# Kernel tuning notes

Measured on AMD Instinct MI355X. Metric: run time of the kernel, lower is better.

The kernel has to match this reference:

```python
import jax, jax.numpy as jnp
import numpy as np

NEG_BIG = -9e15
LRELU_SLOPE = 0.2  # alpha

N = 8192
IN_F = 256
OUT_F = 128


def setup_inputs() -> dict:
    key = jax.random.key(0)
    k1, k2, k3, k4 = jax.random.split(key, 4)
    inputs = jax.random.normal(k1, (N, IN_F), dtype=jnp.float32)
    adj = jax.random.randint(k2, (N, N), 0, 2, dtype=jnp.int32)
    # xavier_uniform with gain=1.414
    gain = 1.414
    bW = gain * np.sqrt(6.0 / (IN_F + OUT_F))
    W = jax.random.uniform(k3, (IN_F, OUT_F), minval=-bW, maxval=bW, dtype=jnp.float32)
    ba = gain * np.sqrt(6.0 / (2 * OUT_F + 1))
    a = jax.random.uniform(k4, (2 * OUT_F, 1), minval=-ba, maxval=ba, dtype=jnp.float32)
    return {"inputs": inputs, "adj": adj, "W": W, "a": a}


def reference(inputs, adj, W, a):
    # h: [N, F']
    h = inputs @ W
    # a^T [h_i || h_j] = h_i . a[:F'] + h_j . a[F':]  -- avoids the O(N^2 * 2F') concat
    a1 = a[:OUT_F, 0]   # [F']
    a2 = a[OUT_F:, 0]   # [F']
    s1 = h @ a1         # [N]
    s2 = h @ a2         # [N]
    e = s1[:, None] + s2[None, :]                      # [N, N]
    e = jnp.where(e >= 0, e, LRELU_SLOPE * e)          # LeakyReLU(alpha)
    scores = jnp.where(adj > 0, e, jnp.float32(NEG_BIG))
    attention = jax.nn.softmax(scores, axis=1)         # row softmax; dropout p=0
    h_prime = attention @ h                            # [N, F']
    return jax.nn.elu(h_prime)                         # concat=True -> elu
```

## Files before the change

### kernel.cpp

```cpp
#include <hip/hip_runtime.h>
#include <hip/hip_bf16.h>

#define NN   8192
#define INF_ 256
#define OUTF 128
#define SLOPE 0.2f
#define NJC  4
#define JCHUNK (NN / NJC)
#define NT   (JCHUNK / 128)

typedef float f32x4  __attribute__((ext_vector_type(4)));
typedef float f32x16 __attribute__((ext_vector_type(16)));
typedef short bf16x8 __attribute__((ext_vector_type(8)));
typedef int   i32x4  __attribute__((ext_vector_type(4)));
typedef unsigned int u32;
typedef unsigned short u16;
typedef u16 u16x4 __attribute__((ext_vector_type(4)));

__device__ __forceinline__ u16 f2bf(float f) {
  return __builtin_bit_cast(u16, __float2bfloat16(f));
}


__global__ __launch_bounds__(256) void gat_k0(const int* __restrict__ adj,
                                              unsigned char* __restrict__ bm) {
  const int idx = blockIdx.x * 256 + threadIdx.x;
  const int r  = idx >> 10;
  const int jg = idx & 1023;
  const int* p = adj + (size_t)r * NN + jg * 8;
  i32x4 a0 = *(const i32x4*)p;
  i32x4 a1 = *(const i32x4*)(p + 4);
  unsigned b = 0;
#pragma unroll
  for (int e = 0; e < 4; e++) b |= (a0[e] > 0 ? 1u : 0u) << e;
#pragma unroll
  for (int e = 0; e < 4; e++) b |= (a1[e] > 0 ? 1u : 0u) << (e + 4);
  bm[(size_t)r * 1024 + jg] = (unsigned char)b;
}

__global__ __launch_bounds__(256) void gat_k1(
    const float* __restrict__ X, const float* __restrict__ W,
    const float* __restrict__ a, u16* __restrict__ hbF,
    float* __restrict__ s1, float* __restrict__ s2) {
  __shared__ float xs[32 * INF_];
  const int t = threadIdx.x;
  const int r0 = blockIdx.x * 32;
  {
    const f32x4* src = (const f32x4*)(X + (size_t)r0 * INF_);
    f32x4* dst = (f32x4*)xs;
    for (int i = t; i < 32 * INF_ / 4; i += 256) dst[i] = src[i];
  }
  __syncthreads();
  const int cg = t & 31;
  const int rg = t >> 5;
  float acc[4][4];
#pragma unroll
  for (int i = 0; i < 4; i++)
#pragma unroll
    for (int j = 0; j < 4; j++) acc[i][j] = 0.f;

  for (int k = 0; k < INF_; k += 4) {
    f32x4 xv[4];
#pragma unroll
    for (int i = 0; i < 4; i++) xv[i] = *(const f32x4*)&xs[(rg * 4 + i) * INF_ + k];
#pragma unroll
    for (int kk = 0; kk < 4; kk++) {
      f32x4 wv = *(const f32x4*)&W[(k + kk) * OUTF + cg * 4];
#pragma unroll
      for (int i = 0; i < 4; i++)
#pragma unroll
        for (int j = 0; j < 4; j++) acc[i][j] = fmaf(xv[i][kk], wv[j], acc[i][j]);
    }
  }

  f32x4 a1v = *(const f32x4*)&a[cg * 4];
  f32x4 a2v = *(const f32x4*)&a[OUTF + cg * 4];
  float p1[4], p2[4];
#pragma unroll
  for (int i = 0; i < 4; i++) {
    p1[i] = acc[i][0] * a1v[0] + acc[i][1] * a1v[1] + acc[i][2] * a1v[2] + acc[i][3] * a1v[3];
    p2[i] = acc[i][0] * a2v[0] + acc[i][1] * a2v[1] + acc[i][2] * a2v[2] + acc[i][3] * a2v[3];
  }
#pragma unroll
  for (int m = 1; m < 32; m <<= 1) {
#pragma unroll
    for (int i = 0; i < 4; i++) {
      p1[i] += __shfl_xor(p1[i], m);
      p2[i] += __shfl_xor(p2[i], m);
    }
  }
  if (cg == 0) {
#pragma unroll
    for (int i = 0; i < 4; i++) {
      s1[r0 + rg * 4 + i] = p1[i];
      s2[r0 + rg * 4 + i] = p2[i];
    }
  }

  const int R0 = r0 + rg * 4;
  const int jg = (R0 & 2047) >> 3;
  const int tt = jg & 15;
  const int pr = jg >> 4;
  const int wq = pr >> 1;
  const int gg = pr & 1;
  const int e0 = R0 & 7;
  const int n  = ((R0 >> 11) * 16 + tt) * 8 + wq;
#pragma unroll
  for (int j = 0; j < 4; j++) {
    const int C = cg * 4 + j;
    u16x4 pk;
#pragma unroll
    for (int i = 0; i < 4; i++) pk[i] = f2bf(acc[i][j]);
    size_t flat = ((size_t)(n * 4 + (C >> 5)) * 64 + (C & 31) + 32 * gg) * 8 + e0;
    *(u16x4*)(hbF + flat) = pk;
  }
}

__global__ __launch_bounds__(1024) void gat_k2(const float* __restrict__ s2,
                                               float* __restrict__ s2m,
                                               float* __restrict__ E1,
                                               float* __restrict__ E2) {
  __shared__ float sm[16];
  const int t = threadIdx.x;
  float m = -1e30f;
  for (int i = t; i < NN / 4; i += 1024) {
    f32x4 v = ((const f32x4*)s2)[i];
    f32x4 e1, e2;
#pragma unroll
    for (int k = 0; k < 4; k++) {
      m = fmaxf(m, v[k]);
      e1[k] = __expf(v[k]);
      e2[k] = __expf(SLOPE * v[k]);
    }
    ((f32x4*)E1)[i] = e1;
    ((f32x4*)E2)[i] = e2;
  }
#pragma unroll
  for (int k = 1; k < 64; k <<= 1) m = fmaxf(m, __shfl_xor(m, k));
  if ((t & 63) == 0) sm[t >> 6] = m;
  __syncthreads();
  if (t == 0) {
    float mm = sm[0];
#pragma unroll
    for (int k = 1; k < 16; k++) mm = fmaxf(mm, sm[k]);
    *s2m = mm;
  }
}

__device__ __forceinline__ void st16(float* dst, const f32x16& A, int g) {
#pragma unroll
  for (int r = 0; r < 16; r++) {
    const int dr = (r & 3) + 8 * (r >> 2) + 4 * g;
    dst[dr * 128] = A[r];
  }
}
__device__ __forceinline__ void ad16(float* dst, const f32x16& A, int g) {
#pragma unroll
  for (int r = 0; r < 16; r++) {
    const int dr = (r & 3) + 8 * (r >> 2) + 4 * g;
    dst[dr * 128] += A[r];
  }
}

__global__ __launch_bounds__(512, 4) void gat_k3(
    const unsigned char* __restrict__ bm, const u16* __restrict__ hbF,
    const float* __restrict__ s1g, const float* __restrict__ E1,
    const float* __restrict__ E2, const float* __restrict__ s2maxp,
    float* __restrict__ part, float* __restrict__ dpart) {
  __shared__ float lred[8192];
  __shared__ float dred[256];
  const int t = threadIdx.x;
  const int w = t >> 6;
  const int l = t & 63;
  const int rb = blockIdx.x & 255;
  const int jc = blockIdx.x >> 8;
  const int r0 = rb * 32;
  const int row = l & 31;
  const int g = l >> 5;

  const float s1r = s1g[r0 + row];
  const float s2m = *s2maxp;
  float Mi = s1r + s2m;
  Mi = fmaxf(Mi, SLOPE * Mi);
  const float A = __expf(s1r - Mi);
  const float B = __expf(SLOPE * s1r - Mi);

  const int pr = 2 * w + g;
  const i32x4 bmv = *(const i32x4*)(bm + (size_t)(r0 + row) * 1024 +
                                    jc * 256 + pr * 16);

  f32x16 acc0 = 0.f, acc1 = 0.f, acc2 = 0.f, acc3 = 0.f;

  const float* e1p = E1 + jc * JCHUNK + pr * 128;
  const float* e2p = E2 + jc * JCHUNK + pr * 128;
  const bf16x8* bp = (const bf16x8*)hbF + ((size_t)(jc * 128 + w) * 4) * 64 + l;

  float dsA = 0.f, dsB = 0.f;
#pragma unroll
  for (int q4 = 0; q4 < 4; q4++) {
    const unsigned word = (unsigned)bmv[q4];
#pragma unroll
    for (int ti = 0; ti < 4; ti++) {
      const int tt = q4 * 4 + ti;
      const unsigned b = word >> (ti * 8);
      const bf16x8* bq = bp + (size_t)tt * 2048;
      bf16x8 b0 = bq[0], b1 = bq[64], b2 = bq[128], b3 = bq[192];
      f32x4 u0 = *(const f32x4*)(e1p + 8 * tt);
      f32x4 u1 = *(const f32x4*)(e1p + 8 * tt + 4);
      f32x4 v0 = *(const f32x4*)(e2p + 8 * tt);
      f32x4 v1 = *(const f32x4*)(e2p + 8 * tt + 4);
      const float uu[8] = {u0[0], u0[1], u0[2], u0[3], u1[0], u1[1], u1[2], u1[3]};
      const float vv[8] = {v0[0], v0[1], v0[2], v0[3], v1[0], v1[1], v1[2], v1[3]};

      u32 aw[4];
#pragma unroll
      for (int e = 0; e < 8; e += 2) {
        float pa = fmaxf(A * uu[e],     B * vv[e]);
        float pb = fmaxf(A * uu[e + 1], B * vv[e + 1]);
        pa = (b & (1u << e))       ? pa : 0.f;
        pb = (b & (1u << (e + 1))) ? pb : 0.f;
        dsA += pa;
        dsB += pb;
        aw[e >> 1] = __builtin_amdgcn_perm(
            __builtin_bit_cast(u32, pb) + 0x8000u,
            __builtin_bit_cast(u32, pa) + 0x8000u, 0x07060302u);
      }
      const bf16x8 af =
          __builtin_bit_cast(bf16x8, (i32x4){(int)aw[0], (int)aw[1],
                                             (int)aw[2], (int)aw[3]});
      acc0 = __builtin_amdgcn_mfma_f32_32x32x16_bf16(af, b0, acc0, 0, 0, 0);
      acc1 = __builtin_amdgcn_mfma_f32_32x32x16_bf16(af, b1, acc1, 0, 0, 0);
      acc2 = __builtin_amdgcn_mfma_f32_32x32x16_bf16(af, b2, acc2, 0, 0, 0);
      acc3 = __builtin_amdgcn_mfma_f32_32x32x16_bf16(af, b3, acc3, 0, 0, 0);
    }
  }
  float dsum = dsA + dsB;

  dsum += __shfl_xor(dsum, 32);
  if (l < 32) dred[w * 32 + l] = dsum;

  const int colw = l & 31;
  if (w < 2) {
    st16(&lred[w * 4096 + 0 * 32 + colw], acc0, g);
    st16(&lred[w * 4096 + 1 * 32 + colw], acc1, g);
    st16(&lred[w * 4096 + 2 * 32 + colw], acc2, g);
    st16(&lred[w * 4096 + 3 * 32 + colw], acc3, g);
  }
  __syncthreads();
  if (t < 32) {
    float d = 0.f;
#pragma unroll
    for (int w8 = 0; w8 < 8; w8++) d += dred[w8 * 32 + t];
    dpart[jc * NN + r0 + t] = d;
  }
  if (w == 2 || w == 3) {
    ad16(&lred[(w - 2) * 4096 + 0 * 32 + colw], acc0, g);
    ad16(&lred[(w - 2) * 4096 + 1 * 32 + colw], acc1, g);
    ad16(&lred[(w - 2) * 4096 + 2 * 32 + colw], acc2, g);
    ad16(&lred[(w - 2) * 4096 + 3 * 32 + colw], acc3, g);
  }
  __syncthreads();
  if (w == 4 || w == 5) {
    ad16(&lred[(w - 4) * 4096 + 0 * 32 + colw], acc0, g);
    ad16(&lred[(w - 4) * 4096 + 1 * 32 + colw], acc1, g);
    ad16(&lred[(w - 4) * 4096 + 2 * 32 + colw], acc2, g);
    ad16(&lred[(w - 4) * 4096 + 3 * 32 + colw], acc3, g);
  }
  __syncthreads();
  if (w == 6 || w == 7) {
    ad16(&lred[(w - 6) * 4096 + 0 * 32 + colw], acc0, g);
    ad16(&lred[(w - 6) * 4096 + 1 * 32 + colw], acc1, g);
    ad16(&lred[(w - 6) * 4096 + 2 * 32 + colw], acc2, g);
    ad16(&lred[(w - 6) * 4096 + 3 * 32 + colw], acc3, g);
  }
  __syncthreads();

  const int flat = t * 8;
  f32x4 pa = *(f32x4*)&lred[flat];
  f32x4 pb = *(f32x4*)&lred[flat + 4];
  pa += *(f32x4*)&lred[4096 + flat];
  pb += *(f32x4*)&lred[4096 + flat + 4];
  float* pp = part + (size_t)jc * (NN * OUTF) + (size_t)r0 * OUTF + flat;
  *(f32x4*)pp = pa;
  *(f32x4*)(pp + 4) = pb;
}

__global__ __launch_bounds__(256) void gat_k4(
    const float* __restrict__ part, const float* __restrict__ dpart,
    float* __restrict__ out) {
  const int idx = blockIdx.x * 256 + threadIdx.x;
  const int e4 = idx * 4;
  const int i = e4 >> 7;
  f32x4 p = {0.f, 0.f, 0.f, 0.f};
  float d = 0.f;
#pragma unroll
  for (int jc = 0; jc < NJC; jc++) {
    p += *(const f32x4*)&part[(size_t)jc * (NN * OUTF) + e4];
    d += dpart[jc * NN + i];
  }
  d = fmaxf(d, 1e-30f);
  f32x4 r;
#pragma unroll
  for (int k = 0; k < 4; k++) {
    float v = p[k] / d;
    r[k] = (v > 0.f) ? v : expm1f(v);
  }
  *(f32x4*)&out[e4] = r;
}

extern "C" void kernel_launch(void* const* d_in, const int* in_sizes, int n_in,
                              void* d_out, int out_size, void* d_ws, size_t ws_size,
                              hipStream_t stream) {
  (void)in_sizes; (void)n_in; (void)out_size; (void)ws_size;
  const float* X  = (const float*)d_in[0];
  const int*  adj = (const int*)d_in[1];
  const float* W  = (const float*)d_in[2];
  const float* a  = (const float*)d_in[3];
  float* out = (float*)d_out;

  char* ws = (char*)d_ws;
  u16*   hbF   = (u16*)ws;
  float* s1    = (float*)(ws + (2u << 20));
  float* s2    = (float*)(ws + (2u << 20) + (32u << 10));
  float* s2m   = (float*)(ws + (2u << 20) + (64u << 10));
  float* E1    = (float*)(ws + (2u << 20) + (128u << 10));
  float* E2    = (float*)(ws + (2u << 20) + (160u << 10));
  float* dpart = (float*)(ws + (2u << 20) + (192u << 10));
  unsigned char* bm = (unsigned char*)(ws + (3u << 20));
  float* part  = (float*)(ws + (12u << 20));

  gat_k0<<<NN * 1024 / 256, 256, 0, stream>>>(adj, bm);
  gat_k1<<<NN / 32, 256, 0, stream>>>(X, W, a, hbF, s1, s2);
  gat_k2<<<1, 1024, 0, stream>>>(s2, s2m, E1, E2);
  gat_k3<<<256 * NJC, 512, 0, stream>>>(bm, hbF, s1, E1, E2, s2m, part, dpart);
  gat_k4<<<(NN * OUTF / 4) / 256, 256, 0, stream>>>(part, dpart, out);
}
```

Before: 114.1 us.

## Process 64 rows per block in attention kernel to reuse loaded h tiles

Each gat_k3 block now handles two 32-row groups instead of one. The same bf16 h fragments and E1/E2 values are reused for both groups' MFMAs, halving the global loads of h per row. The grid is halved to 512 blocks and the launch-bounds occupancy hint drops to 1, which doubles accumulator registers per thread. This lowers occupancy, may reduce latency hiding across the device, and adds a second LDS reduction pass.

```diff
diff --git a/kernel.cpp b/kernel.cpp
--- a/kernel.cpp
+++ b/kernel.cpp
@@ -162,47 +162,53 @@
   }
 }
 
-__global__ __launch_bounds__(512, 4) void gat_k3(
+__global__ __launch_bounds__(512, 1) void gat_k3(
     const unsigned char* __restrict__ bm, const u16* __restrict__ hbF,
     const float* __restrict__ s1g, const float* __restrict__ E1,
     const float* __restrict__ E2, const float* __restrict__ s2maxp,
     float* __restrict__ part, float* __restrict__ dpart) {
   __shared__ float lred[8192];
-  __shared__ float dred[256];
+  __shared__ float dred[512];
   const int t = threadIdx.x;
   const int w = t >> 6;
   const int l = t & 63;
-  const int rb = blockIdx.x & 255;
-  const int jc = blockIdx.x >> 8;
-  const int r0 = rb * 32;
+  const int rb = blockIdx.x & 127;
+  const int jc = blockIdx.x >> 7;
+  const int r0 = rb * 64;
   const int row = l & 31;
   const int g = l >> 5;
 
-  const float s1r = s1g[r0 + row];
   const float s2m = *s2maxp;
-  float Mi = s1r + s2m;
-  Mi = fmaxf(Mi, SLOPE * Mi);
-  const float A = __expf(s1r - Mi);
-  const float B = __expf(SLOPE * s1r - Mi);
+  const float s1r0 = s1g[r0 + row];
+  const float s1r1 = s1g[r0 + 32 + row];
+  float Mi0 = s1r0 + s2m; Mi0 = fmaxf(Mi0, SLOPE * Mi0);
+  float Mi1 = s1r1 + s2m; Mi1 = fmaxf(Mi1, SLOPE * Mi1);
+  const float A0 = __expf(s1r0 - Mi0), B0 = __expf(SLOPE * s1r0 - Mi0);
+  const float A1 = __expf(s1r1 - Mi1), B1 = __expf(SLOPE * s1r1 - Mi1);
 
   const int pr = 2 * w + g;
-  const i32x4 bmv = *(const i32x4*)(bm + (size_t)(r0 + row) * 1024 +
-                                    jc * 256 + pr * 16);
-
-  f32x16 acc0 = 0.f, acc1 = 0.f, acc2 = 0.f, acc3 = 0.f;
+  const i32x4 bmv0 = *(const i32x4*)(bm + (size_t)(r0 + row) * 1024 +
+                                     jc * 256 + pr * 16);
+  const i32x4 bmv1 = *(const i32x4*)(bm + (size_t)(r0 + 32 + row) * 1024 +
+                                     jc * 256 + pr * 16);
+
+  f32x16 a00 = 0.f, a01 = 0.f, a02 = 0.f, a03 = 0.f;
+  f32x16 a10 = 0.f, a11 = 0.f, a12 = 0.f, a13 = 0.f;
 
   const float* e1p = E1 + jc * JCHUNK + pr * 128;
   const float* e2p = E2 + jc * JCHUNK + pr * 128;
   const bf16x8* bp = (const bf16x8*)hbF + ((size_t)(jc * 128 + w) * 4) * 64 + l;
 
-  float dsA = 0.f, dsB = 0.f;
+  float dsA0 = 0.f, dsB0 = 0.f, dsA1 = 0.f, dsB1 = 0.f;
 #pragma unroll
   for (int q4 = 0; q4 < 4; q4++) {
-    const unsigned word = (unsigned)bmv[q4];
+    const unsigned w0 = (unsigned)bmv0[q4];
+    const unsigned w1 = (unsigned)bmv1[q4];
 #pragma unroll
     for (int ti = 0; ti < 4; ti++) {
       const int tt = q4 * 4 + ti;
-      const unsigned b = word >> (ti * 8);
+      const unsigned b0m = w0 >> (ti * 8);
+      const unsigned b1m = w1 >> (ti * 8);
       const bf16x8* bq = bp + (size_t)tt * 2048;
       bf16x8 b0 = bq[0], b1 = bq[64], b2 = bq[128], b3 = bq[192];
       f32x4 u0 = *(const f32x4*)(e1p + 8 * tt);
@@ -212,77 +218,136 @@
       const float uu[8] = {u0[0], u0[1], u0[2], u0[3], u1[0], u1[1], u1[2], u1[3]};
       const float vv[8] = {v0[0], v0[1], v0[2], v0[3], v1[0], v1[1], v1[2], v1[3]};
 
-      u32 aw[4];
+      u32 aw0[4], aw1[4];
 #pragma unroll
       for (int e = 0; e < 8; e += 2) {
-        float pa = fmaxf(A * uu[e],     B * vv[e]);
-        float pb = fmaxf(A * uu[e + 1], B * vv[e + 1]);
-        pa = (b & (1u << e))       ? pa : 0.f;
-        pb = (b & (1u << (e + 1))) ? pb : 0.f;
-        dsA += pa;
-        dsB += pb;
-        aw[e >> 1] = __builtin_amdgcn_perm(
-            __builtin_bit_cast(u32, pb) + 0x8000u,
-            __builtin_bit_cast(u32, pa) + 0x8000u, 0x07060302u);
+        float pa0 = fmaxf(A0 * uu[e],     B0 * vv[e]);
+        float pb0 = fmaxf(A0 * uu[e + 1], B0 * vv[e + 1]);
+        pa0 = (b0m & (1u << e))       ? pa0 : 0.f;
+        pb0 = (b0m & (1u << (e + 1))) ? pb0 : 0.f;
+        dsA0 += pa0; dsB0 += pb0;
+        aw0[e >> 1] = __builtin_amdgcn_perm(
+            __builtin_bit_cast(u32, pb0) + 0x8000u,
+            __builtin_bit_cast(u32, pa0) + 0x8000u, 0x07060302u);
+        float pa1 = fmaxf(A1 * uu[e],     B1 * vv[e]);
+        float pb1 = fmaxf(A1 * uu[e + 1], B1 * vv[e + 1]);
+        pa1 = (b1m & (1u << e))       ? pa1 : 0.f;
+        pb1 = (b1m & (1u << (e + 1))) ? pb1 : 0.f;
+        dsA1 += pa1; dsB1 += pb1;
+        aw1[e >> 1] = __builtin_amdgcn_perm(
+            __builtin_bit_cast(u32, pb1) + 0x8000u,
+            __builtin_bit_cast(u32, pa1) + 0x8000u, 0x07060302u);
       }
-      const bf16x8 af =
-          __builtin_bit_cast(bf16x8, (i32x4){(int)aw[0], (int)aw[1],
-                                             (int)aw[2], (int)aw[3]});
-      acc0 = __builtin_amdgcn_mfma_f32_32x32x16_bf16(af, b0, acc0, 0, 0, 0);
-      acc1 = __builtin_amdgcn_mfma_f32_32x32x16_bf16(af, b1, acc1, 0, 0, 0);
-      acc2 = __builtin_amdgcn_mfma_f32_32x32x16_bf16(af, b2, acc2, 0, 0, 0);
-      acc3 = __builtin_amdgcn_mfma_f32_32x32x16_bf16(af, b3, acc3, 0, 0, 0);
+      const bf16x8 af0 = __builtin_bit_cast(
+          bf16x8, (i32x4){(int)aw0[0], (int)aw0[1], (int)aw0[2], (int)aw0[3]});
+      const bf16x8 af1 = __builtin_bit_cast(
+          bf16x8, (i32x4){(int)aw1[0], (int)aw1[1], (int)aw1[2], (int)aw1[3]});
+      a00 = __builtin_amdgcn_mfma_f32_32x32x16_bf16(af0, b0, a00, 0, 0, 0);
+      a10 = __builtin_amdgcn_mfma_f32_32x32x16_bf16(af1, b0, a10, 0, 0, 0);
+      a01 = __builtin_amdgcn_mfma_f32_32x32x16_bf16(af0, b1, a01, 0, 0, 0);
+      a11 = __builtin_amdgcn_mfma_f32_32x32x16_bf16(af1, b1, a11, 0, 0, 0);
+      a02 = __builtin_amdgcn_mfma_f32_32x32x16_bf16(af0, b2, a02, 0, 0, 0);
+      a12 = __builtin_amdgcn_mfma_f32_32x32x16_bf16(af1, b2, a12, 0, 0, 0);
+      a03 = __builtin_amdgcn_mfma_f32_32x32x16_bf16(af0, b3, a03, 0, 0, 0);
+      a13 = __builtin_amdgcn_mfma_f32_32x32x16_bf16(af1, b3, a13, 0, 0, 0);
     }
   }
-  float dsum = dsA + dsB;
-
-  dsum += __shfl_xor(dsum, 32);
-  if (l < 32) dred[w * 32 + l] = dsum;
+  float dsum0 = dsA0 + dsB0;
+  float dsum1 = dsA1 + dsB1;
+
+  dsum0 += __shfl_xor(dsum0, 32);
+  dsum1 += __shfl_xor(dsum1, 32);
+  if (l < 32) {
+    dred[w * 64 + l] = dsum0;
+    dred[w * 64 + 32 + l] = dsum1;
+  }
 
   const int colw = l & 31;
+  const int flat = t * 8;
+
   if (w < 2) {
-    st16(&lred[w * 4096 + 0 * 32 + colw], acc0, g);
-    st16(&lred[w * 4096 + 1 * 32 + colw], acc1, g);
-    st16(&lred[w * 4096 + 2 * 32 + colw], acc2, g);
-    st16(&lred[w * 4096 + 3 * 32 + colw], acc3, g);
-  }
-  __syncthreads();
-  if (t < 32) {
+    st16(&lred[w * 4096 + 0 * 32 + colw], a00, g);
+    st16(&lred[w * 4096 + 1 * 32 + colw], a01, g);
+    st16(&lred[w * 4096 + 2 * 32 + colw], a02, g);
+    st16(&lred[w * 4096 + 3 * 32 + colw], a03, g);
+  }
+  __syncthreads();
+  if (t < 64) {
     float d = 0.f;
 #pragma unroll
-    for (int w8 = 0; w8 < 8; w8++) d += dred[w8 * 32 + t];
+    for (int w8 = 0; w8 < 8; w8++) d += dred[w8 * 64 + t];
     dpart[jc * NN + r0 + t] = d;
   }
   if (w == 2 || w == 3) {
-    ad16(&lred[(w - 2) * 4096 + 0 * 32 + colw], acc0, g);
-    ad16(&lred[(w - 2) * 4096 + 1 * 32 + colw], acc1, g);
-    ad16(&lred[(w - 2) * 4096 + 2 * 32 + colw], acc2, g);
-    ad16(&lred[(w - 2) * 4096 + 3 * 32 + colw], acc3, g);
+    ad16(&lred[(w - 2) * 4096 + 0 * 32 + colw], a00, g);
+    ad16(&lred[(w - 2) * 4096 + 1 * 32 + colw], a01, g);
+    ad16(&lred[(w - 2) * 4096 + 2 * 32 + colw], a02, g);
+    ad16(&lred[(w - 2) * 4096 + 3 * 32 + colw], a03, g);
   }
   __syncthreads();
   if (w == 4 || w == 5) {
-    ad16(&lred[(w - 4) * 4096 + 0 * 32 + colw], acc0, g);
-    ad16(&lred[(w - 4) * 4096 + 1 * 32 + colw], acc1, g);
-    ad16(&lred[(w - 4) * 4096 + 2 * 32 + colw], acc2, g);
-    ad16(&lred[(w - 4) * 4096 + 3 * 32 + colw], acc3, g);
+    ad16(&lred[(w - 4) * 4096 + 0 * 32 + colw], a00, g);
+    ad16(&lred[(w - 4) * 4096 + 1 * 32 + colw], a01, g);
+    ad16(&lred[(w - 4) * 4096 + 2 * 32 + colw], a02, g);
+    ad16(&lred[(w - 4) * 4096 + 3 * 32 + colw], a03, g);
   }
   __syncthreads();
   if (w == 6 || w == 7) {
-    ad16(&lred[(w - 6) * 4096 + 0 * 32 + colw], acc0, g);
-    ad16(&lred[(w - 6) * 4096 + 1 * 32 + colw], acc1, g);
-    ad16(&lred[(w - 6) * 4096 + 2 * 32 + colw], acc2, g);
-    ad16(&lred[(w - 6) * 4096 + 3 * 32 + colw], acc3, g);
-  }
-  __syncthreads();
-
-  const int flat = t * 8;
-  f32x4 pa = *(f32x4*)&lred[flat];
-  f32x4 pb = *(f32x4*)&lred[flat + 4];
-  pa += *(f32x4*)&lred[4096 + flat];
-  pb += *(f32x4*)&lred[4096 + flat + 4];
-  float* pp = part + (size_t)jc * (NN * OUTF) + (size_t)r0 * OUTF + flat;
-  *(f32x4*)pp = pa;
-  *(f32x4*)(pp + 4) = pb;
+    ad16(&lred[(w - 6) * 4096 + 0 * 32 + colw], a00, g);
+    ad16(&lred[(w - 6) * 4096 + 1 * 32 + colw], a01, g);
+    ad16(&lred[(w - 6) * 4096 + 2 * 32 + colw], a02, g);
+    ad16(&lred[(w - 6) * 4096 + 3 * 32 + colw], a03, g);
+  }
+  __syncthreads();
+  {
+    f32x4 pa = *(f32x4*)&lred[flat];
+    f32x4 pb = *(f32x4*)&lred[flat + 4];
+    pa += *(f32x4*)&lred[4096 + flat];
+    pb += *(f32x4*)&lred[4096 + flat + 4];
+    float* pp = part + (size_t)jc * (NN * OUTF) + (size_t)r0 * OUTF + flat;
+    *(f32x4*)pp = pa;
+    *(f32x4*)(pp + 4) = pb;
+  }
+  __syncthreads();
+
+  if (w < 2) {
+    st16(&lred[w * 4096 + 0 * 32 + colw], a10, g);
+    st16(&lred[w * 4096 + 1 * 32 + colw], a11, g);
+    st16(&lred[w * 4096 + 2 * 32 + colw], a12, g);
+    st16(&lred[w * 4096 + 3 * 32 + colw], a13, g);
+  }
+  __syncthreads();
+  if (w == 2 || w == 3) {
+    ad16(&lred[(w - 2) * 4096 + 0 * 32 + colw], a10, g);
+    ad16(&lred[(w - 2) * 4096 + 1 * 32 + colw], a11, g);
+    ad16(&lred[(w - 2) * 4096 + 2 * 32 + colw], a12, g);
+    ad16(&lred[(w - 2) * 4096 + 3 * 32 + colw], a13, g);
+  }
+  __syncthreads();
+  if (w == 4 || w == 5) {
+    ad16(&lred[(w - 4) * 4096 + 0 * 32 + colw], a10, g);
+    ad16(&lred[(w - 4) * 4096 + 1 * 32 + colw], a11, g);
+    ad16(&lred[(w - 4) * 4096 + 2 * 32 + colw], a12, g);
+    ad16(&lred[(w - 4) * 4096 + 3 * 32 + colw], a13, g);
+  }
+  __syncthreads();
+  if (w == 6 || w == 7) {
+    ad16(&lred[(w - 6) * 4096 + 0 * 32 + colw], a10, g);
+    ad16(&lred[(w - 6) * 4096 + 1 * 32 + colw], a11, g);
+    ad16(&lred[(w - 6) * 4096 + 2 * 32 + colw], a12, g);
+    ad16(&lred[(w - 6) * 4096 + 3 * 32 + colw], a13, g);
+  }
+  __syncthreads();
+  {
+    f32x4 pa = *(f32x4*)&lred[flat];
+    f32x4 pb = *(f32x4*)&lred[flat + 4];
+    pa += *(f32x4*)&lred[4096 + flat];
+    pb += *(f32x4*)&lred[4096 + flat + 4];
+    float* pp = part + (size_t)jc * (NN * OUTF) +
+                (size_t)(r0 + 32) * OUTF + flat;
+    *(f32x4*)pp = pa;
+    *(f32x4*)(pp + 4) = pb;
+  }
 }
 
 __global__ __launch_bounds__(256) void gat_k4(
@@ -332,6 +397,6 @@
   gat_k0<<<NN * 1024 / 256, 256, 0, stream>>>(adj, bm);
   gat_k1<<<NN / 32, 256, 0, stream>>>(X, W, a, hbF, s1, s2);
   gat_k2<<<1, 1024, 0, stream>>>(s2, s2m, E1, E2);
-  gat_k3<<<256 * NJC, 512, 0, stream>>>(bm, hbF, s1, E1, E2, s2m, part, dpart);
+  gat_k3<<<128 * NJC, 512, 0, stream>>>(bm, hbF, s1, E1, E2, s2m, part, dpart);
   gat_k4<<<(NN * OUTF / 4) / 256, 256, 0, stream>>>(part, dpart, out);
 }
```

Result: no change. 113.0 us (-0.9%).

## Fuse adjacency bitmask packing into attention kernel and parallelize max reduction

Applied to the files above, without the earlier changes.

Removes the separate pass that packed the int32 adjacency matrix into a bitmask in global memory. Each attention block now reads its own 32-row by 2048-column adjacency tile, packs it into bits in shared memory (reusing the reduction buffer), and syncs before the main loop. The single-block max/exp kernel is split across 8 blocks that each write a partial max, and the attention kernel reduces those 8 values itself. This drops one launch plus the bitmask write and re-read, at the cost of an extra prologue and two barriers in the attention kernel.

```diff
diff --git a/kernel.cpp b/kernel.cpp
--- a/kernel.cpp
+++ b/kernel.cpp
@@ -21,22 +21,6 @@
   return __builtin_bit_cast(u16, __float2bfloat16(f));
 }
 
-
-__global__ __launch_bounds__(256) void gat_k0(const int* __restrict__ adj,
-                                              unsigned char* __restrict__ bm) {
-  const int idx = blockIdx.x * 256 + threadIdx.x;
-  const int r  = idx >> 10;
-  const int jg = idx & 1023;
-  const int* p = adj + (size_t)r * NN + jg * 8;
-  i32x4 a0 = *(const i32x4*)p;
-  i32x4 a1 = *(const i32x4*)(p + 4);
-  unsigned b = 0;
-#pragma unroll
-  for (int e = 0; e < 4; e++) b |= (a0[e] > 0 ? 1u : 0u) << e;
-#pragma unroll
-  for (int e = 0; e < 4; e++) b |= (a1[e] > 0 ? 1u : 0u) << (e + 4);
-  bm[(size_t)r * 1024 + jg] = (unsigned char)b;
-}
 
 __global__ __launch_bounds__(256) void gat_k1(
     const float* __restrict__ X, const float* __restrict__ W,
@@ -116,35 +100,30 @@
   }
 }
 
-__global__ __launch_bounds__(1024) void gat_k2(const float* __restrict__ s2,
-                                               float* __restrict__ s2m,
-                                               float* __restrict__ E1,
-                                               float* __restrict__ E2) {
-  __shared__ float sm[16];
+__global__ __launch_bounds__(256) void gat_k2(const float* __restrict__ s2,
+                                              float* __restrict__ bmax,
+                                              float* __restrict__ E1,
+                                              float* __restrict__ E2) {
+  __shared__ float sm[4];
   const int t = threadIdx.x;
+  const int i = blockIdx.x * 256 + t;
+  f32x4 v = ((const f32x4*)s2)[i];
+  f32x4 e1, e2;
   float m = -1e30f;
-  for (int i = t; i < NN / 4; i += 1024) {
-    f32x4 v = ((const f32x4*)s2)[i];
-    f32x4 e1, e2;
-#pragma unroll
-    for (int k = 0; k < 4; k++) {
-      m = fmaxf(m, v[k]);
-      e1[k] = __expf(v[k]);
-      e2[k] = __expf(SLOPE * v[k]);
-    }
-    ((f32x4*)E1)[i] = e1;
-    ((f32x4*)E2)[i] = e2;
-  }
+#pragma unroll
+  for (int k = 0; k < 4; k++) {
+    m = fmaxf(m, v[k]);
+    e1[k] = __expf(v[k]);
+    e2[k] = __expf(SLOPE * v[k]);
+  }
+  ((f32x4*)E1)[i] = e1;
+  ((f32x4*)E2)[i] = e2;
 #pragma unroll
   for (int k = 1; k < 64; k <<= 1) m = fmaxf(m, __shfl_xor(m, k));
   if ((t & 63) == 0) sm[t >> 6] = m;
   __syncthreads();
-  if (t == 0) {
-    float mm = sm[0];
-#pragma unroll
-    for (int k = 1; k < 16; k++) mm = fmaxf(mm, sm[k]);
-    *s2m = mm;
-  }
+  if (t == 0)
+    bmax[blockIdx.x] = fmaxf(fmaxf(sm[0], sm[1]), fmaxf(sm[2], sm[3]));
 }
 
 __device__ __forceinline__ void st16(float* dst, const f32x16& A, int g) {
@@ -163,9 +142,9 @@
 }
 
 __global__ __launch_bounds__(512, 4) void gat_k3(
-    const unsigned char* __restrict__ bm, const u16* __restrict__ hbF,
+    const int* __restrict__ adj, const u16* __restrict__ hbF,
     const float* __restrict__ s1g, const float* __restrict__ E1,
-    const float* __restrict__ E2, const float* __restrict__ s2maxp,
+    const float* __restrict__ E2, const float* __restrict__ bmax,
     float* __restrict__ part, float* __restrict__ dpart) {
   __shared__ float lred[8192];
   __shared__ float dred[256];
@@ -178,16 +157,37 @@
   const int row = l & 31;
   const int g = l >> 5;
 
+  unsigned char* bits = (unsigned char*)lred;
+  {
+    const int prow = t >> 4;
+    const int cl = t & 15;
+    const int* ap = adj + (size_t)(r0 + prow) * NN + jc * JCHUNK + cl * 8;
+#pragma unroll 4
+    for (int k = 0; k < 16; k++) {
+      i32x4 x0 = *(const i32x4*)(ap + k * 128);
+      i32x4 x1 = *(const i32x4*)(ap + k * 128 + 4);
+      unsigned b = 0;
+#pragma unroll
+      for (int e = 0; e < 4; e++) b |= (x0[e] > 0 ? 1u : 0u) << e;
+#pragma unroll
+      for (int e = 0; e < 4; e++) b |= (x1[e] > 0 ? 1u : 0u) << (e + 4);
+      bits[prow * 256 + k * 16 + cl] = (unsigned char)b;
+    }
+  }
+  __syncthreads();
+
+  float s2m = bmax[0];
+#pragma unroll
+  for (int k = 1; k < 8; k++) s2m = fmaxf(s2m, bmax[k]);
   const float s1r = s1g[r0 + row];
-  const float s2m = *s2maxp;
   float Mi = s1r + s2m;
   Mi = fmaxf(Mi, SLOPE * Mi);
   const float A = __expf(s1r - Mi);
   const float B = __expf(SLOPE * s1r - Mi);
 
   const int pr = 2 * w + g;
-  const i32x4 bmv = *(const i32x4*)(bm + (size_t)(r0 + row) * 1024 +
-                                    jc * 256 + pr * 16);
+  const i32x4 bmv = *(const i32x4*)(bits + row * 256 + pr * 16);
+  __syncthreads();
 
   f32x16 acc0 = 0.f, acc1 = 0.f, acc2 = 0.f, acc3 = 0.f;
 
@@ -322,16 +322,14 @@
   u16*   hbF   = (u16*)ws;
   float* s1    = (float*)(ws + (2u << 20));
   float* s2    = (float*)(ws + (2u << 20) + (32u << 10));
-  float* s2m   = (float*)(ws + (2u << 20) + (64u << 10));
+  float* bmax  = (float*)(ws + (2u << 20) + (64u << 10));
   float* E1    = (float*)(ws + (2u << 20) + (128u << 10));
   float* E2    = (float*)(ws + (2u << 20) + (160u << 10));
   float* dpart = (float*)(ws + (2u << 20) + (192u << 10));
-  unsigned char* bm = (unsigned char*)(ws + (3u << 20));
-  float* part  = (float*)(ws + (12u << 20));
-
-  gat_k0<<<NN * 1024 / 256, 256, 0, stream>>>(adj, bm);
+  float* part  = (float*)(ws + (4u << 20));
+
   gat_k1<<<NN / 32, 256, 0, stream>>>(X, W, a, hbF, s1, s2);
-  gat_k2<<<1, 1024, 0, stream>>>(s2, s2m, E1, E2);
-  gat_k3<<<256 * NJC, 512, 0, stream>>>(bm, hbF, s1, E1, E2, s2m, part, dpart);
+  gat_k2<<<8, 256, 0, stream>>>(s2, bmax, E1, E2);
+  gat_k3<<<256 * NJC, 512, 0, stream>>>(adj, hbF, s1, E1, E2, bmax, part, dpart);
   gat_k4<<<(NN * OUTF / 4) / 256, 256, 0, stream>>>(part, dpart, out);
 }
```

After: 103.2 us. 1.11x faster.
